# Optimization experiments

Hardware: AMD Instinct MI355X
Metric: run time of the kernel (lower is better)

The kernel has to match this reference:

```python
import jax, jax.numpy as jnp
import numpy as np

D_MODEL = 256
N_HEADS = 4
D_FF = 512
LN_EPS = 1e-5


def _ln(x, g, b):
    mu = jnp.mean(x, axis=-1, keepdims=True)
    var = jnp.mean(jnp.square(x - mu), axis=-1, keepdims=True)
    return (x - mu) * jax.lax.rsqrt(var + LN_EPS) * g + b


def setup_inputs() -> dict:
    key = jax.random.key(0)
    ks = jax.random.split(key, 12)
    d, h, f = D_MODEL, N_HEADS, D_FF
    s = 0.02
    return {
        "x": jax.random.normal(ks[0], (8, 2048, d), jnp.float32),
        # per-head Q/K/V projections: each head maps d_model -> d_model
        "Wq": jax.random.normal(ks[1], (h, d, d), jnp.float32) * s,
        "bq": jnp.zeros((h, d), jnp.float32),
        "Wk": jax.random.normal(ks[2], (h, d, d), jnp.float32) * s,
        "bk": jnp.zeros((h, d), jnp.float32),
        "Wv": jax.random.normal(ks[3], (h, d, d), jnp.float32) * s,
        "bv": jnp.zeros((h, d), jnp.float32),
        # output projection: (n_heads*d_model) -> d_model
        "Wo": jax.random.normal(ks[4], (h * d, d), jnp.float32) * s,
        "bo": jnp.zeros((d,), jnp.float32),
        # LayerNorms
        "g1": jnp.ones((d,), jnp.float32),
        "be1": jnp.zeros((d,), jnp.float32),
        "g2": jnp.ones((d,), jnp.float32),
        "be2": jnp.zeros((d,), jnp.float32),
        # FFN
        "W1": jax.random.normal(ks[5], (d, f), jnp.float32) * s,
        "bf1": jnp.zeros((f,), jnp.float32),
        "W2": jax.random.normal(ks[6], (f, d), jnp.float32) * s,
        "bf2": jnp.zeros((d,), jnp.float32),
    }


def reference(x, Wq, bq, Wk, bk, Wv, bv, Wo, bo, g1, be1, g2, be2, W1, bf1, W2, bf2):
    # Pre-norm attention block (dropout is identity at inference)
    xn = _ln(x, g1, be1)  # [b,s,d]
    q = jnp.einsum("bsd,hde->bhse", xn, Wq) + bq[None, :, None, :]
    k = jnp.einsum("bsd,hde->bhse", xn, Wk) + bk[None, :, None, :]
    v = jnp.einsum("bsd,hde->bhse", xn, Wv) + bv[None, :, None, :]
    scale = q.shape[-1] ** -0.5  # per-head dim == d_model here
    scores = jax.nn.softmax(jnp.einsum("bhse,bhte->bhst", q, k) * scale, axis=-1)
    attn = jnp.einsum("bhst,bhte->bhse", scores, v)  # [b,h,s,d]
    b, h, s, d = attn.shape
    cat = jnp.transpose(attn, (0, 2, 1, 3)).reshape(b, s, h * d)  # concat heads
    x = x + cat @ Wo + bo
    # Pre-norm FFN block
    xn = _ln(x, g2, be2)
    x = x + jax.nn.relu(xn @ W1 + bf1) @ W2 + bf2
    return x
```

## Files before the change

kernel.cpp:

```cpp
#include <hip/hip_runtime.h>

typedef __bf16 bf16x8 __attribute__((ext_vector_type(8)));
typedef float  f32x4  __attribute__((ext_vector_type(4)));
typedef float  f32x16 __attribute__((ext_vector_type(16)));

__device__ __forceinline__ unsigned short f2b(float f) {
    union { float f; unsigned int v; } c; c.f = f;
    unsigned int u = c.v;
    unsigned int r = u + 0x7FFFu + ((u >> 16) & 1u);
    return (unsigned short)(r >> 16);
}
__device__ __forceinline__ f32x4 mfma16(bf16x8 a, bf16x8 b, f32x4 c) {
    return __builtin_amdgcn_mfma_f32_16x16x32_bf16(a, b, c, 0, 0, 0);
}
__device__ __forceinline__ f32x16 mfma32(bf16x8 a, bf16x8 b, f32x16 c) {
    return __builtin_amdgcn_mfma_f32_32x32x16_bf16(a, b, c, 0, 0, 0);
}
__device__ __forceinline__ unsigned cvtpk(float a, float b) {
    unsigned r;
    asm("v_cvt_pk_bf16_f32 %0, %1, %2" : "=v"(r) : "v"(a), "v"(b));
    return r;
}

#define BB 8
#define SS 2048
#define DD 256
#define HH 4
#define FF 512
#define MM (BB * SS)

__global__ __launch_bounds__(256) void transpose_f32_kernel(
    const float* __restrict__ in, unsigned short* __restrict__ out,
    int inS, int outS, long long inZa, long long inZb, int zmod, long long outZ,
    float scale)
{
    __shared__ unsigned short T[64][72];
    const int z = blockIdx.z;
    in  += (long long)(z / zmod) * inZa + (long long)(z % zmod) * inZb;
    out += (long long)z * outZ;
    const int r0 = blockIdx.x * 64, c0 = blockIdx.y * 64;
    const int tid = threadIdx.x;
    const int row = tid >> 3;
    const int col = (tid & 7) * 8;
#pragma unroll
    for (int c = 0; c < 2; ++c) {
        int rr = c * 32 + row;
        const float4 a = *reinterpret_cast<const float4*>(&in[(long long)(r0 + rr) * inS + c0 + col]);
        const float4 b = *reinterpret_cast<const float4*>(&in[(long long)(r0 + rr) * inS + c0 + col + 4]);
        alignas(16) unsigned short t[8] = {
            f2b(a.x * scale), f2b(a.y * scale), f2b(a.z * scale), f2b(a.w * scale),
            f2b(b.x * scale), f2b(b.y * scale), f2b(b.z * scale), f2b(b.w * scale) };
        *reinterpret_cast<uint4*>(&T[rr][col]) = *reinterpret_cast<const uint4*>(t);
    }
    __syncthreads();
#pragma unroll
    for (int c = 0; c < 2; ++c) {
        int orow = c * 32 + row;
        alignas(16) unsigned short tmp[8];
#pragma unroll
        for (int j = 0; j < 8; ++j) tmp[j] = T[col + j][orow];
        *reinterpret_cast<uint4*>(&out[(long long)(c0 + orow) * outS + r0 + col]) =
            *reinterpret_cast<const uint4*>(tmp);
    }
}

__global__ __launch_bounds__(256) void bias_concat_kernel(
    const float* __restrict__ bq, const float* __restrict__ bk,
    const float* __restrict__ bv, float* __restrict__ qkb, float* __restrict__ vb)
{
    const int i = blockIdx.x * 256 + threadIdx.x;
    if (i < 1024)       qkb[i] = bq[i] * 0.0625f;
    else if (i < 2048)  qkb[i] = bk[i - 1024];
    else                vb[i - 2048] = bv[i - 2048];
}

__global__ __launch_bounds__(256) void ln_kernel(
    const float* __restrict__ in, const float* __restrict__ g,
    const float* __restrict__ bta, unsigned short* __restrict__ out)
{
    const int tid  = threadIdx.x;
    const int wave = tid >> 6, lane = tid & 63;
    const int row  = blockIdx.x * 4 + wave;
    const float4 v = reinterpret_cast<const float4*>(in)[(long long)row * 64 + lane];
    float x[4] = { v.x, v.y, v.z, v.w };
    float s = x[0] + x[1] + x[2] + x[3];
    float q = x[0]*x[0] + x[1]*x[1] + x[2]*x[2] + x[3]*x[3];
#pragma unroll
    for (int off = 1; off < 64; off <<= 1) {
        s += __shfl_xor(s, off);
        q += __shfl_xor(q, off);
    }
    const float mean = s * (1.0f / 256.0f);
    const float var  = q * (1.0f / 256.0f) - mean * mean;
    const float rs   = rsqrtf(var + 1e-5f);
    const float4 gv = reinterpret_cast<const float4*>(g)[lane];
    const float4 bv = reinterpret_cast<const float4*>(bta)[lane];
    unsigned short y[4];
    y[0] = f2b((x[0] - mean) * rs * gv.x + bv.x);
    y[1] = f2b((x[1] - mean) * rs * gv.y + bv.y);
    y[2] = f2b((x[2] - mean) * rs * gv.z + bv.z);
    y[3] = f2b((x[3] - mean) * rs * gv.w + bv.w);
    uint2 o;
    o.x = (unsigned int)y[0] | ((unsigned int)y[1] << 16);
    o.y = (unsigned int)y[2] | ((unsigned int)y[3] << 16);
    reinterpret_cast<uint2*>(out)[(long long)row * 64 + lane] = o;
}

template <bool RELU, int RES, bool OUTBF, int NS, bool VT>
__global__ __launch_bounds__(256) void gemm_kernel(
    const unsigned short* __restrict__ A, const unsigned short* __restrict__ BT,
    const float* __restrict__ bias, const float* __restrict__ res,
    void* __restrict__ out, int M, int N, int K)
{
    __shared__ unsigned short As[128 * 40];
    __shared__ unsigned short Bs[(NS == 4 ? 128 : 64) * 40];
    const int tid  = threadIdx.x;
    const int wave = tid >> 6, lane = tid & 63;
    const int quad = lane >> 4, l16 = lane & 15;
    const int wm = wave >> 1, wn = wave & 1;
    const int WN = NS * 16;
    const int m0 = blockIdx.x * 128, n0 = blockIdx.y * (2 * WN);

    f32x4 acc[4][NS];
#pragma unroll
    for (int i = 0; i < 4; ++i)
#pragma unroll
        for (int j = 0; j < NS; ++j) acc[i][j] = (f32x4){0.f, 0.f, 0.f, 0.f};

    const int srow = tid >> 2;
    const int scol = (tid & 3) * 8;

    for (int k0 = 0; k0 < K; k0 += 32) {
        __syncthreads();
#pragma unroll
        for (int c = 0; c < 2; ++c) {
            const int r = c * 64 + srow;
            *reinterpret_cast<uint4*>(&As[r * 40 + scol]) =
                *reinterpret_cast<const uint4*>(&A[(long long)(m0 + r) * K + k0 + scol]);
        }
        {
            *reinterpret_cast<uint4*>(&Bs[srow * 40 + scol]) =
                *reinterpret_cast<const uint4*>(&BT[(long long)(n0 + srow) * K + k0 + scol]);
            if (NS == 4) {
                const int r = 64 + srow;
                *reinterpret_cast<uint4*>(&Bs[r * 40 + scol]) =
                    *reinterpret_cast<const uint4*>(&BT[(long long)(n0 + r) * K + k0 + scol]);
            }
        }
        __syncthreads();
        bf16x8 af[4], bf[NS];
#pragma unroll
        for (int ms = 0; ms < 4; ++ms)
            af[ms] = *reinterpret_cast<const bf16x8*>(&As[(wm * 64 + ms * 16 + l16) * 40 + quad * 8]);
#pragma unroll
        for (int ns = 0; ns < NS; ++ns)
            bf[ns] = *reinterpret_cast<const bf16x8*>(&Bs[(wn * WN + ns * 16 + l16) * 40 + quad * 8]);
#pragma unroll
        for (int ms = 0; ms < 4; ++ms)
#pragma unroll
            for (int ns = 0; ns < NS; ++ns)
                acc[ms][ns] = mfma16(af[ms], bf[ns], acc[ms][ns]);
    }

#pragma unroll
    for (int ms = 0; ms < 4; ++ms) {
#pragma unroll
        for (int ns = 0; ns < NS; ++ns) {
            const int cg = n0 + wn * WN + ns * 16 + l16;
            const float bvc = VT ? 0.f : bias[cg];
#pragma unroll
            for (int r = 0; r < 4; ++r) {
                const int rg = m0 + wm * 64 + ms * 16 + quad * 4 + r;
                float v = acc[ms][ns][r] + (VT ? bias[rg] : bvc);
                if (RELU)   v = fmaxf(v, 0.0f);
                if (RES == 1)
                    v += res[(long long)rg * N + cg];
                if (VT) {
                    const long long oaddr =
                        (long long)((cg >> 11) * 4 + (rg >> 8)) * 524288 +
                        (long long)(rg & 255) * 2048 + (cg & 2047);
                    reinterpret_cast<unsigned short*>(out)[oaddr] = f2b(v);
                } else if (OUTBF) {
                    reinterpret_cast<unsigned short*>(out)[(long long)rg * N + cg] = f2b(v);
                } else {
                    reinterpret_cast<float*>(out)[(long long)rg * N + cg] = v;
                }
            }
        }
    }
}

__global__ __launch_bounds__(256, 2) void attn_kernel(
    const unsigned short* __restrict__ QK, const unsigned short* __restrict__ Vt,
    unsigned short* __restrict__ Cat)
{
    __shared__ __align__(16) unsigned short Ks[2][32 * 264];
    __shared__ __align__(16) unsigned short Vs[2][256 * 40];
    const int tid  = threadIdx.x;
    const int wave = tid >> 6, lane = tid & 63;
    const int l32 = lane & 31, half = lane >> 5;
    const int by = blockIdx.x;
    const int h = by & 3, b = by >> 2;
    const int q0 = blockIdx.y * 128;
    const unsigned short* Qb = QK + (long long)b * SS * 2048 + h * 256;
    const unsigned short* Kb = Qb + 1024;
    const unsigned short* vbase = Vt + (long long)by * DD * SS;

    bf16x8 qf[16];
    {
        const unsigned short* qrow = Qb + (long long)(q0 + wave * 32 + l32) * 2048 + half * 8;
#pragma unroll
        for (int kb = 0; kb < 16; ++kb)
            qf[kb] = *reinterpret_cast<const bf16x8*>(qrow + kb * 16);
    }

    f32x16 o[8];
#pragma unroll
    for (int i = 0; i < 8; ++i)
#pragma unroll
        for (int r = 0; r < 16; ++r) o[i][r] = 0.f;
    float lsum = 0.f;

    const int krow = tid >> 3;
    const int kcol = (tid & 7) * 8;
    const int ve   = tid >> 2;
    const int vtf  = (tid & 3) * 8;

    uint4 kreg[4], vreg[4];
#pragma unroll
    for (int c = 0; c < 4; ++c)
        kreg[c] = *reinterpret_cast<const uint4*>(&Kb[(long long)krow * 2048 + kcol + c * 64]);
#pragma unroll
    for (int c = 0; c < 4; ++c)
        vreg[c] = *reinterpret_cast<const uint4*>(&vbase[(long long)(ve + c * 64) * SS + vtf]);
#pragma unroll
    for (int c = 0; c < 4; ++c)
        *reinterpret_cast<uint4*>(&Ks[0][krow * 264 + kcol + c * 64]) = kreg[c];
#pragma unroll
    for (int c = 0; c < 4; ++c)
        *reinterpret_cast<uint4*>(&Vs[0][(ve + c * 64) * 40 + vtf]) = vreg[c];
    __syncthreads();

    for (int t = 0; t < 64; ++t) {
        const int cur = t & 1;
        if (t < 63) {
            const int t1 = (t + 1) * 32;
#pragma unroll
            for (int c = 0; c < 4; ++c)
                kreg[c] = *reinterpret_cast<const uint4*>(&Kb[(long long)(t1 + krow) * 2048 + kcol + c * 64]);
#pragma unroll
            for (int c = 0; c < 4; ++c)
                vreg[c] = *reinterpret_cast<const uint4*>(&vbase[(long long)(ve + c * 64) * SS + t1 + vtf]);
        }

        f32x16 sc0, sc1;
#pragma unroll
        for (int r = 0; r < 16; ++r) { sc0[r] = 0.f; sc1[r] = 0.f; }
        __builtin_amdgcn_s_setprio(1);
#pragma unroll
        for (int kb = 0; kb < 8; ++kb) {
            bf16x8 kf0 = *reinterpret_cast<const bf16x8*>(&Ks[cur][l32 * 264 + (2 * kb) * 16 + half * 8]);
            bf16x8 kf1 = *reinterpret_cast<const bf16x8*>(&Ks[cur][l32 * 264 + (2 * kb + 1) * 16 + half * 8]);
            sc0 = mfma32(kf0, qf[2 * kb], sc0);
            sc1 = mfma32(kf1, qf[2 * kb + 1], sc1);
        }
        __builtin_amdgcn_s_setprio(0);

        float p[16];
#pragma unroll
        for (int r = 0; r < 16; ++r) {
            p[r] = __expf(sc0[r] + sc1[r]);
            lsum += p[r];
        }

        unsigned pk[8];
#pragma unroll
        for (int i = 0; i < 8; ++i) pk[i] = cvtpk(p[2 * i], p[2 * i + 1]);
        union { bf16x8 v; unsigned u[4]; } A0, A1;
        {
            auto r = __builtin_amdgcn_permlane32_swap(pk[0], pk[2], false, false);
            A0.u[0] = r[0]; A0.u[2] = r[1];
        }
        {
            auto r = __builtin_amdgcn_permlane32_swap(pk[1], pk[3], false, false);
            A0.u[1] = r[0]; A0.u[3] = r[1];
        }
        {
            auto r = __builtin_amdgcn_permlane32_swap(pk[4], pk[6], false, false);
            A1.u[0] = r[0]; A1.u[2] = r[1];
        }
        {
            auto r = __builtin_amdgcn_permlane32_swap(pk[5], pk[7], false, false);
            A1.u[1] = r[0]; A1.u[3] = r[1];
        }

        __builtin_amdgcn_s_setprio(1);
#pragma unroll
        for (int et = 0; et < 8; ++et) {
            bf16x8 vf0 = *reinterpret_cast<const bf16x8*>(&Vs[cur][(et * 32 + l32) * 40 + half * 8]);
            bf16x8 vf1 = *reinterpret_cast<const bf16x8*>(&Vs[cur][(et * 32 + l32) * 40 + 16 + half * 8]);
            o[et] = mfma32(A0.v, vf0, o[et]);
            o[et] = mfma32(A1.v, vf1, o[et]);
        }
        __builtin_amdgcn_s_setprio(0);

        if (t < 63) {
            const int nxt = cur ^ 1;
#pragma unroll
            for (int c = 0; c < 4; ++c)
                *reinterpret_cast<uint4*>(&Ks[nxt][krow * 264 + kcol + c * 64]) = kreg[c];
#pragma unroll
            for (int c = 0; c < 4; ++c)
                *reinterpret_cast<uint4*>(&Vs[nxt][(ve + c * 64) * 40 + vtf]) = vreg[c];
            __syncthreads();
        }
    }

    lsum += __shfl_xor(lsum, 32);
    const float inv = 1.0f / lsum;
    float invr[16];
#pragma unroll
    for (int r = 0; r < 16; ++r)
        invr[r] = __shfl(inv, (r & 3) + 8 * (r >> 2) + 4 * half);

    const int rowb = b * SS + q0 + wave * 32;
#pragma unroll
    for (int et = 0; et < 8; ++et) {
        const int cg = h * 256 + et * 32 + l32;
#pragma unroll
        for (int r = 0; r < 16; ++r) {
            const int row = (r & 3) + 8 * (r >> 2) + 4 * half;
            Cat[(long long)(rowb + row) * (HH * DD) + cg] = f2b(o[et][r] * invr[r]);
        }
    }
}

extern "C" void kernel_launch(void* const* d_in, const int* in_sizes, int n_in,
                              void* d_out, int out_size, void* d_ws, size_t ws_size,
                              hipStream_t stream)
{
    const float* x   = (const float*)d_in[0];
    const float* Wq  = (const float*)d_in[1];
    const float* bq  = (const float*)d_in[2];
    const float* Wk  = (const float*)d_in[3];
    const float* bk  = (const float*)d_in[4];
    const float* Wv  = (const float*)d_in[5];
    const float* bv  = (const float*)d_in[6];
    const float* Wo  = (const float*)d_in[7];
    const float* bo  = (const float*)d_in[8];
    const float* g1  = (const float*)d_in[9];
    const float* be1 = (const float*)d_in[10];
    const float* g2  = (const float*)d_in[11];
    const float* be2 = (const float*)d_in[12];
    const float* W1  = (const float*)d_in[13];
    const float* bf1 = (const float*)d_in[14];
    const float* W2  = (const float*)d_in[15];
    const float* bf2 = (const float*)d_in[16];
    float* out = (float*)d_out;

    char* ws = (char*)d_ws;
    unsigned short* xn1  = (unsigned short*)(ws + 0);
    unsigned short* qk   = (unsigned short*)(ws + 8388608);
    unsigned short* cat  = (unsigned short*)(ws + 75497472);
    unsigned short* vt   = (unsigned short*)(ws + 109051904);
    unsigned short* wqkT = (unsigned short*)(ws + 142606336);
    unsigned short* wvT  = (unsigned short*)(ws + 143654912);
    unsigned short* woT  = (unsigned short*)(ws + 144179200);
    unsigned short* w1T  = (unsigned short*)(ws + 144703488);
    unsigned short* w2T  = (unsigned short*)(ws + 144965632);
    float*          qkb  = (float*)(ws + 145227776);
    float*          vb   = (float*)(ws + 145235968);
    float*          xmid = (float*)(ws + 8388608);
    unsigned short* xn2  = (unsigned short*)(ws + 25165824);
    unsigned short* mid  = (unsigned short*)(ws + 33554432);

    transpose_f32_kernel<<<dim3(4, 4, 4),  256, 0, stream>>>(Wq, wqkT,          256,  256, 0, 65536, 4, 65536, 0.0625f);
    transpose_f32_kernel<<<dim3(4, 4, 4),  256, 0, stream>>>(Wk, wqkT + 262144, 256,  256, 0, 65536, 4, 65536, 1.0f);
    transpose_f32_kernel<<<dim3(4, 4, 4),  256, 0, stream>>>(Wv, wvT,           256,  256, 0, 65536, 4, 65536, 1.0f);
    transpose_f32_kernel<<<dim3(16, 4, 1), 256, 0, stream>>>(Wo, woT,           256, 1024, 0, 0, 4, 0, 1.0f);
    transpose_f32_kernel<<<dim3(4, 8, 1),  256, 0, stream>>>(W1, w1T,           512,  256, 0, 0, 4, 0, 1.0f);
    transpose_f32_kernel<<<dim3(8, 4, 1),  256, 0, stream>>>(W2, w2T,           256,  512, 0, 0, 4, 0, 1.0f);
    bias_concat_kernel<<<dim3(12), 256, 0, stream>>>(bq, bk, bv, qkb, vb);

    ln_kernel<<<dim3(4096), 256, 0, stream>>>(x, g1, be1, xn1);

    gemm_kernel<false, 0, true, 4, false><<<dim3(128, 16), 256, 0, stream>>>(
        xn1, wqkT, qkb, nullptr, qk, MM, 2048, 256);
    gemm_kernel<false, 0, true, 4, true><<<dim3(8, 128), 256, 0, stream>>>(
        wvT, xn1, vb, nullptr, vt, 1024, MM, 256);

    attn_kernel<<<dim3(32, 16), 256, 0, stream>>>(qk, vt, cat);

    gemm_kernel<false, 1, false, 2, false><<<dim3(128, 4), 256, 0, stream>>>(
        cat, woT, bo, x, xmid, MM, 256, 1024);

    ln_kernel<<<dim3(4096), 256, 0, stream>>>(xmid, g2, be2, xn2);

    gemm_kernel<true, 0, true, 2, false><<<dim3(128, 8), 256, 0, stream>>>(
        xn2, w1T, bf1, nullptr, mid, MM, 512, 256);

    gemm_kernel<false, 1, false, 2, false><<<dim3(128, 4), 256, 0, stream>>>(
        mid, w2T, bf2, xmid, out, MM, 256, 512);

    (void)in_sizes; (void)n_in; (void)out_size; (void)ws_size;
}
```

Baseline: 363.4 us.

## Software-pipeline attention QK^T one tile ahead and fold log2e into Q scale

Restructures the attention key loop so the score MMA for tile t+1 is issued before the softmax and PV MMA of tile t. Two score accumulators alternate, the loop is unrolled by two with a macro, and global prefetch now runs two tiles ahead. The Q weights and bias are also prescaled by log2(e) so exp2f replaces __expf. The aim is to overlap exp/convert/permute work with MFMA and LDS latency, at the cost of more registers and a restructured barrier placement.

```diff
diff --git a/kernel.cpp b/kernel.cpp
--- a/kernel.cpp
+++ b/kernel.cpp
@@ -28,6 +28,7 @@
 #define HH 4
 #define FF 512
 #define MM (BB * SS)
+#define QSCALE (0.0625f * 1.44269504088896340736f)
 
 __global__ __launch_bounds__(256) void transpose_f32_kernel(
     const float* __restrict__ in, unsigned short* __restrict__ out,
@@ -69,7 +70,7 @@
     const float* __restrict__ bv, float* __restrict__ qkb, float* __restrict__ vb)
 {
     const int i = blockIdx.x * 256 + threadIdx.x;
-    if (i < 1024)       qkb[i] = bq[i] * 0.0625f;
+    if (i < 1024)       qkb[i] = bq[i] * QSCALE;
     else if (i < 2048)  qkb[i] = bk[i - 1024];
     else                vb[i - 2048] = bv[i - 2048];
 }
@@ -241,79 +242,103 @@
         *reinterpret_cast<uint4*>(&Vs[0][(ve + c * 64) * 40 + vtf]) = vreg[c];
     __syncthreads();
 
-    for (int t = 0; t < 64; ++t) {
-        const int cur = t & 1;
-        if (t < 63) {
-            const int t1 = (t + 1) * 32;
-#pragma unroll
-            for (int c = 0; c < 4; ++c)
-                kreg[c] = *reinterpret_cast<const uint4*>(&Kb[(long long)(t1 + krow) * 2048 + kcol + c * 64]);
-#pragma unroll
-            for (int c = 0; c < 4; ++c)
-                vreg[c] = *reinterpret_cast<const uint4*>(&vbase[(long long)(ve + c * 64) * SS + t1 + vtf]);
-        }
-
-        f32x16 sc0, sc1;
-#pragma unroll
-        for (int r = 0; r < 16; ++r) { sc0[r] = 0.f; sc1[r] = 0.f; }
+    f32x16 scA, scB;
+    {
+#pragma unroll
+        for (int r = 0; r < 16; ++r) scA[r] = 0.f;
         __builtin_amdgcn_s_setprio(1);
 #pragma unroll
-        for (int kb = 0; kb < 8; ++kb) {
-            bf16x8 kf0 = *reinterpret_cast<const bf16x8*>(&Ks[cur][l32 * 264 + (2 * kb) * 16 + half * 8]);
-            bf16x8 kf1 = *reinterpret_cast<const bf16x8*>(&Ks[cur][l32 * 264 + (2 * kb + 1) * 16 + half * 8]);
-            sc0 = mfma32(kf0, qf[2 * kb], sc0);
-            sc1 = mfma32(kf1, qf[2 * kb + 1], sc1);
+        for (int kb = 0; kb < 16; ++kb) {
+            bf16x8 kf = *reinterpret_cast<const bf16x8*>(&Ks[0][l32 * 264 + kb * 16 + half * 8]);
+            scA = mfma32(kf, qf[kb], scA);
         }
         __builtin_amdgcn_s_setprio(0);
-
+#pragma unroll
+        for (int c = 0; c < 4; ++c)
+            kreg[c] = *reinterpret_cast<const uint4*>(&Kb[(long long)(32 + krow) * 2048 + kcol + c * 64]);
+#pragma unroll
+        for (int c = 0; c < 4; ++c)
+            vreg[c] = *reinterpret_cast<const uint4*>(&vbase[(long long)(ve + c * 64) * SS + 32 + vtf]);
+    }
+
+#define ATTN_BODY(SCC, SCN, T, CUR, NXT)                                                        \
+    {                                                                                           \
+        _Pragma("unroll")                                                                       \
+        for (int c = 0; c < 4; ++c)                                                             \
+            *reinterpret_cast<uint4*>(&Ks[NXT][krow * 264 + kcol + c * 64]) = kreg[c];          \
+        __syncthreads();                                                                        \
+        _Pragma("unroll")                                                                       \
+        for (int c = 0; c < 4; ++c)                                                             \
+            *reinterpret_cast<uint4*>(&Vs[NXT][(ve + c * 64) * 40 + vtf]) = vreg[c];            \
+        _Pragma("unroll")                                                                       \
+        for (int r = 0; r < 16; ++r) SCN[r] = 0.f;                                              \
+        __builtin_amdgcn_s_setprio(1);                                                          \
+        _Pragma("unroll")                                                                       \
+        for (int kb = 0; kb < 16; ++kb) {                                                       \
+            bf16x8 kf = *reinterpret_cast<const bf16x8*>(&Ks[NXT][l32 * 264 + kb * 16 + half * 8]); \
+            SCN = mfma32(kf, qf[kb], SCN);                                                      \
+        }                                                                                       \
+        __builtin_amdgcn_s_setprio(0);                                                          \
+        float p[16];                                                                            \
+        _Pragma("unroll")                                                                       \
+        for (int r = 0; r < 16; ++r) { p[r] = exp2f(SCC[r]); lsum += p[r]; }                    \
+        unsigned pk[8];                                                                         \
+        _Pragma("unroll")                                                                       \
+        for (int i = 0; i < 8; ++i) pk[i] = cvtpk(p[2 * i], p[2 * i + 1]);                      \
+        union { bf16x8 v; unsigned u[4]; } A0, A1;                                              \
+        { auto rr = __builtin_amdgcn_permlane32_swap(pk[0], pk[2], false, false); A0.u[0] = rr[0]; A0.u[2] = rr[1]; } \
+        { auto rr = __builtin_amdgcn_permlane32_swap(pk[1], pk[3], false, false); A0.u[1] = rr[0]; A0.u[3] = rr[1]; } \
+        { auto rr = __builtin_amdgcn_permlane32_swap(pk[4], pk[6], false, false); A1.u[0] = rr[0]; A1.u[2] = rr[1]; } \
+        { auto rr = __builtin_amdgcn_permlane32_swap(pk[5], pk[7], false, false); A1.u[1] = rr[0]; A1.u[3] = rr[1]; } \
+        {                                                                                       \
+            const int t2 = ((T) + 2 <= 63 ? (T) + 2 : 63) * 32;                                 \
+            _Pragma("unroll")                                                                   \
+            for (int c = 0; c < 4; ++c)                                                         \
+                kreg[c] = *reinterpret_cast<const uint4*>(&Kb[(long long)(t2 + krow) * 2048 + kcol + c * 64]); \
+            _Pragma("unroll")                                                                   \
+            for (int c = 0; c < 4; ++c)                                                         \
+                vreg[c] = *reinterpret_cast<const uint4*>(&vbase[(long long)(ve + c * 64) * SS + t2 + vtf]); \
+        }                                                                                       \
+        __builtin_amdgcn_s_setprio(1);                                                          \
+        _Pragma("unroll")                                                                       \
+        for (int et = 0; et < 8; ++et) {                                                        \
+            bf16x8 vf0 = *reinterpret_cast<const bf16x8*>(&Vs[CUR][(et * 32 + l32) * 40 + half * 8]);      \
+            bf16x8 vf1 = *reinterpret_cast<const bf16x8*>(&Vs[CUR][(et * 32 + l32) * 40 + 16 + half * 8]); \
+            o[et] = mfma32(A0.v, vf0, o[et]);                                                   \
+            o[et] = mfma32(A1.v, vf1, o[et]);                                                   \
+        }                                                                                       \
+        __builtin_amdgcn_s_setprio(0);                                                          \
+    }
+
+    for (int t = 0; t < 62; t += 2) {
+        ATTN_BODY(scA, scB, t, 0, 1);
+        ATTN_BODY(scB, scA, t + 1, 1, 0);
+    }
+    ATTN_BODY(scA, scB, 62, 0, 1);
+#undef ATTN_BODY
+
+    __syncthreads();
+    {
         float p[16];
 #pragma unroll
-        for (int r = 0; r < 16; ++r) {
-            p[r] = __expf(sc0[r] + sc1[r]);
-            lsum += p[r];
-        }
-
+        for (int r = 0; r < 16; ++r) { p[r] = exp2f(scB[r]); lsum += p[r]; }
         unsigned pk[8];
 #pragma unroll
         for (int i = 0; i < 8; ++i) pk[i] = cvtpk(p[2 * i], p[2 * i + 1]);
         union { bf16x8 v; unsigned u[4]; } A0, A1;
-        {
-            auto r = __builtin_amdgcn_permlane32_swap(pk[0], pk[2], false, false);
-            A0.u[0] = r[0]; A0.u[2] = r[1];
-        }
-        {
-            auto r = __builtin_amdgcn_permlane32_swap(pk[1], pk[3], false, false);
-            A0.u[1] = r[0]; A0.u[3] = r[1];
-        }
-        {
-            auto r = __builtin_amdgcn_permlane32_swap(pk[4], pk[6], false, false);
-            A1.u[0] = r[0]; A1.u[2] = r[1];
-        }
-        {
-            auto r = __builtin_amdgcn_permlane32_swap(pk[5], pk[7], false, false);
-            A1.u[1] = r[0]; A1.u[3] = r[1];
-        }
-
+        { auto rr = __builtin_amdgcn_permlane32_swap(pk[0], pk[2], false, false); A0.u[0] = rr[0]; A0.u[2] = rr[1]; }
+        { auto rr = __builtin_amdgcn_permlane32_swap(pk[1], pk[3], false, false); A0.u[1] = rr[0]; A0.u[3] = rr[1]; }
+        { auto rr = __builtin_amdgcn_permlane32_swap(pk[4], pk[6], false, false); A1.u[0] = rr[0]; A1.u[2] = rr[1]; }
+        { auto rr = __builtin_amdgcn_permlane32_swap(pk[5], pk[7], false, false); A1.u[1] = rr[0]; A1.u[3] = rr[1]; }
         __builtin_amdgcn_s_setprio(1);
 #pragma unroll
         for (int et = 0; et < 8; ++et) {
-            bf16x8 vf0 = *reinterpret_cast<const bf16x8*>(&Vs[cur][(et * 32 + l32) * 40 + half * 8]);
-            bf16x8 vf1 = *reinterpret_cast<const bf16x8*>(&Vs[cur][(et * 32 + l32) * 40 + 16 + half * 8]);
+            bf16x8 vf0 = *reinterpret_cast<const bf16x8*>(&Vs[1][(et * 32 + l32) * 40 + half * 8]);
+            bf16x8 vf1 = *reinterpret_cast<const bf16x8*>(&Vs[1][(et * 32 + l32) * 40 + 16 + half * 8]);
             o[et] = mfma32(A0.v, vf0, o[et]);
             o[et] = mfma32(A1.v, vf1, o[et]);
         }
         __builtin_amdgcn_s_setprio(0);
-
-        if (t < 63) {
-            const int nxt = cur ^ 1;
-#pragma unroll
-            for (int c = 0; c < 4; ++c)
-                *reinterpret_cast<uint4*>(&Ks[nxt][krow * 264 + kcol + c * 64]) = kreg[c];
-#pragma unroll
-            for (int c = 0; c < 4; ++c)
-                *reinterpret_cast<uint4*>(&Vs[nxt][(ve + c * 64) * 40 + vtf]) = vreg[c];
-            __syncthreads();
-        }
     }
 
     lsum += __shfl_xor(lsum, 32);
@@ -374,7 +399,7 @@
     unsigned short* xn2  = (unsigned short*)(ws + 25165824);
     unsigned short* mid  = (unsigned short*)(ws + 33554432);
 
-    transpose_f32_kernel<<<dim3(4, 4, 4),  256, 0, stream>>>(Wq, wqkT,          256,  256, 0, 65536, 4, 65536, 0.0625f);
+    transpose_f32_kernel<<<dim3(4, 4, 4),  256, 0, stream>>>(Wq, wqkT,          256,  256, 0, 65536, 4, 65536, QSCALE);
     transpose_f32_kernel<<<dim3(4, 4, 4),  256, 0, stream>>>(Wk, wqkT + 262144, 256,  256, 0, 65536, 4, 65536, 1.0f);
     transpose_f32_kernel<<<dim3(4, 4, 4),  256, 0, stream>>>(Wv, wvT,           256,  256, 0, 65536, 4, 65536, 1.0f);
     transpose_f32_kernel<<<dim3(16, 4, 1), 256, 0, stream>>>(Wo, woT,           256, 1024, 0, 0, 4, 0, 1.0f);
```

New measurement: 937.0 us. 2.58x slower.

## Load V fragments directly from global memory and fold log2e into Q scale

Applied to the files above, without the earlier changes.

The attention kernel no longer stages V tiles in shared memory. Each wave reads its V MFMA fragments straight from global memory (the transposed V layout) and interleaves those loads with the PV MFMAs, which removes half the LDS traffic and shared footprint. The log2(e) factor is folded into the Q weight and bias scaling, so the softmax uses exp2f instead of __expf. In exchange, every wave re-reads V from global or L2, so the four waves each fetch the same data, and load latency now sits on the critical path between MFMAs.

```diff
diff --git a/kernel.cpp b/kernel.cpp
--- a/kernel.cpp
+++ b/kernel.cpp
@@ -28,6 +28,7 @@
 #define HH 4
 #define FF 512
 #define MM (BB * SS)
+#define QSCALE (0.0625f * 1.44269504088896340736f)
 
 __global__ __launch_bounds__(256) void transpose_f32_kernel(
     const float* __restrict__ in, unsigned short* __restrict__ out,
@@ -69,7 +70,7 @@
     const float* __restrict__ bv, float* __restrict__ qkb, float* __restrict__ vb)
 {
     const int i = blockIdx.x * 256 + threadIdx.x;
-    if (i < 1024)       qkb[i] = bq[i] * 0.0625f;
+    if (i < 1024)       qkb[i] = bq[i] * QSCALE;
     else if (i < 2048)  qkb[i] = bk[i - 1024];
     else                vb[i - 2048] = bv[i - 2048];
 }
@@ -195,7 +196,6 @@
     unsigned short* __restrict__ Cat)
 {
     __shared__ __align__(16) unsigned short Ks[2][32 * 264];
-    __shared__ __align__(16) unsigned short Vs[2][256 * 40];
     const int tid  = threadIdx.x;
     const int wave = tid >> 6, lane = tid & 63;
     const int l32 = lane & 31, half = lane >> 5;
@@ -223,34 +223,26 @@
 
     const int krow = tid >> 3;
     const int kcol = (tid & 7) * 8;
-    const int ve   = tid >> 2;
-    const int vtf  = (tid & 3) * 8;
-
-    uint4 kreg[4], vreg[4];
+
+#define VLD(ET, O16) (*reinterpret_cast<const bf16x8*>(                                   \
+        &vbase[(long long)((ET) * 32 + l32) * SS + t0 + (O16) + half * 8]))
+
+    uint4 kreg[4];
 #pragma unroll
     for (int c = 0; c < 4; ++c)
         kreg[c] = *reinterpret_cast<const uint4*>(&Kb[(long long)krow * 2048 + kcol + c * 64]);
 #pragma unroll
     for (int c = 0; c < 4; ++c)
-        vreg[c] = *reinterpret_cast<const uint4*>(&vbase[(long long)(ve + c * 64) * SS + vtf]);
-#pragma unroll
-    for (int c = 0; c < 4; ++c)
         *reinterpret_cast<uint4*>(&Ks[0][krow * 264 + kcol + c * 64]) = kreg[c];
-#pragma unroll
-    for (int c = 0; c < 4; ++c)
-        *reinterpret_cast<uint4*>(&Vs[0][(ve + c * 64) * 40 + vtf]) = vreg[c];
     __syncthreads();
 
     for (int t = 0; t < 64; ++t) {
         const int cur = t & 1;
+        const int t0 = t * 32;
         if (t < 63) {
-            const int t1 = (t + 1) * 32;
 #pragma unroll
             for (int c = 0; c < 4; ++c)
-                kreg[c] = *reinterpret_cast<const uint4*>(&Kb[(long long)(t1 + krow) * 2048 + kcol + c * 64]);
-#pragma unroll
-            for (int c = 0; c < 4; ++c)
-                vreg[c] = *reinterpret_cast<const uint4*>(&vbase[(long long)(ve + c * 64) * SS + t1 + vtf]);
+                kreg[c] = *reinterpret_cast<const uint4*>(&Kb[(long long)(t0 + 32 + krow) * 2048 + kcol + c * 64]);
         }
 
         f32x16 sc0, sc1;
@@ -266,42 +258,38 @@
         }
         __builtin_amdgcn_s_setprio(0);
 
-        float p[16];
-#pragma unroll
-        for (int r = 0; r < 16; ++r) {
-            p[r] = __expf(sc0[r] + sc1[r]);
-            lsum += p[r];
-        }
+        bf16x8 va0 = VLD(0, 0), va1 = VLD(0, 16);
+        bf16x8 vb0 = VLD(1, 0), vb1 = VLD(1, 16);
 
         unsigned pk[8];
 #pragma unroll
-        for (int i = 0; i < 8; ++i) pk[i] = cvtpk(p[2 * i], p[2 * i + 1]);
+        for (int i = 0; i < 8; ++i) {
+            const float pa = exp2f(sc0[2 * i]     + sc1[2 * i]);
+            const float pb = exp2f(sc0[2 * i + 1] + sc1[2 * i + 1]);
+            lsum += pa + pb;
+            pk[i] = cvtpk(pa, pb);
+        }
         union { bf16x8 v; unsigned u[4]; } A0, A1;
-        {
-            auto r = __builtin_amdgcn_permlane32_swap(pk[0], pk[2], false, false);
-            A0.u[0] = r[0]; A0.u[2] = r[1];
-        }
-        {
-            auto r = __builtin_amdgcn_permlane32_swap(pk[1], pk[3], false, false);
-            A0.u[1] = r[0]; A0.u[3] = r[1];
-        }
-        {
-            auto r = __builtin_amdgcn_permlane32_swap(pk[4], pk[6], false, false);
-            A1.u[0] = r[0]; A1.u[2] = r[1];
-        }
-        {
-            auto r = __builtin_amdgcn_permlane32_swap(pk[5], pk[7], false, false);
-            A1.u[1] = r[0]; A1.u[3] = r[1];
-        }
+        { auto rr = __builtin_amdgcn_permlane32_swap(pk[0], pk[2], false, false); A0.u[0] = rr[0]; A0.u[2] = rr[1]; }
+        { auto rr = __builtin_amdgcn_permlane32_swap(pk[1], pk[3], false, false); A0.u[1] = rr[0]; A0.u[3] = rr[1]; }
+        { auto rr = __builtin_amdgcn_permlane32_swap(pk[4], pk[6], false, false); A1.u[0] = rr[0]; A1.u[2] = rr[1]; }
+        { auto rr = __builtin_amdgcn_permlane32_swap(pk[5], pk[7], false, false); A1.u[1] = rr[0]; A1.u[3] = rr[1]; }
 
         __builtin_amdgcn_s_setprio(1);
-#pragma unroll
-        for (int et = 0; et < 8; ++et) {
-            bf16x8 vf0 = *reinterpret_cast<const bf16x8*>(&Vs[cur][(et * 32 + l32) * 40 + half * 8]);
-            bf16x8 vf1 = *reinterpret_cast<const bf16x8*>(&Vs[cur][(et * 32 + l32) * 40 + 16 + half * 8]);
-            o[et] = mfma32(A0.v, vf0, o[et]);
-            o[et] = mfma32(A1.v, vf1, o[et]);
-        }
+        o[0] = mfma32(A0.v, va0, o[0]); o[0] = mfma32(A1.v, va1, o[0]);
+        va0 = VLD(2, 0); va1 = VLD(2, 16);
+        o[1] = mfma32(A0.v, vb0, o[1]); o[1] = mfma32(A1.v, vb1, o[1]);
+        vb0 = VLD(3, 0); vb1 = VLD(3, 16);
+        o[2] = mfma32(A0.v, va0, o[2]); o[2] = mfma32(A1.v, va1, o[2]);
+        va0 = VLD(4, 0); va1 = VLD(4, 16);
+        o[3] = mfma32(A0.v, vb0, o[3]); o[3] = mfma32(A1.v, vb1, o[3]);
+        vb0 = VLD(5, 0); vb1 = VLD(5, 16);
+        o[4] = mfma32(A0.v, va0, o[4]); o[4] = mfma32(A1.v, va1, o[4]);
+        va0 = VLD(6, 0); va1 = VLD(6, 16);
+        o[5] = mfma32(A0.v, vb0, o[5]); o[5] = mfma32(A1.v, vb1, o[5]);
+        vb0 = VLD(7, 0); vb1 = VLD(7, 16);
+        o[6] = mfma32(A0.v, va0, o[6]); o[6] = mfma32(A1.v, va1, o[6]);
+        o[7] = mfma32(A0.v, vb0, o[7]); o[7] = mfma32(A1.v, vb1, o[7]);
         __builtin_amdgcn_s_setprio(0);
 
         if (t < 63) {
@@ -309,12 +297,10 @@
 #pragma unroll
             for (int c = 0; c < 4; ++c)
                 *reinterpret_cast<uint4*>(&Ks[nxt][krow * 264 + kcol + c * 64]) = kreg[c];
-#pragma unroll
-            for (int c = 0; c < 4; ++c)
-                *reinterpret_cast<uint4*>(&Vs[nxt][(ve + c * 64) * 40 + vtf]) = vreg[c];
             __syncthreads();
         }
     }
+#undef VLD
 
     lsum += __shfl_xor(lsum, 32);
     const float inv = 1.0f / lsum;
@@ -374,7 +360,7 @@
     unsigned short* xn2  = (unsigned short*)(ws + 25165824);
     unsigned short* mid  = (unsigned short*)(ws + 33554432);
 
-    transpose_f32_kernel<<<dim3(4, 4, 4),  256, 0, stream>>>(Wq, wqkT,          256,  256, 0, 65536, 4, 65536, 0.0625f);
+    transpose_f32_kernel<<<dim3(4, 4, 4),  256, 0, stream>>>(Wq, wqkT,          256,  256, 0, 65536, 4, 65536, QSCALE);
     transpose_f32_kernel<<<dim3(4, 4, 4),  256, 0, stream>>>(Wk, wqkT + 262144, 256,  256, 0, 65536, 4, 65536, 1.0f);
     transpose_f32_kernel<<<dim3(4, 4, 4),  256, 0, stream>>>(Wv, wvT,           256,  256, 0, 65536, 4, 65536, 1.0f);
     transpose_f32_kernel<<<dim3(16, 4, 1), 256, 0, stream>>>(Wo, woT,           256, 1024, 0, 0, 4, 0, 1.0f);
```

New measurement: 504.9 us. 39.0% more time.

## Double-buffer GEMM shared tiles and fold log2e into Q scale for exp2

Applied to the files above, without the earlier changes.

The GEMM kernel now keeps two shared-memory buffers for the A and B tiles. It prefetches the next K-slice into registers while the MFMAs run on the current slice, which leaves one barrier per iteration instead of two. In attention, log2(e) is folded into the Q weight and bias scale so softmax can use exp2f directly. The two split score accumulators are merged into one chain of 16 dependent MFMAs. The double buffering doubles LDS use per block, and the single accumulator chain adds MFMA dependency latency.

```diff
diff --git a/kernel.cpp b/kernel.cpp
--- a/kernel.cpp
+++ b/kernel.cpp
@@ -28,6 +28,7 @@
 #define HH 4
 #define FF 512
 #define MM (BB * SS)
+#define QSCALE (0.0625f * 1.44269504088896340736f)
 
 __global__ __launch_bounds__(256) void transpose_f32_kernel(
     const float* __restrict__ in, unsigned short* __restrict__ out,
@@ -69,7 +70,7 @@
     const float* __restrict__ bv, float* __restrict__ qkb, float* __restrict__ vb)
 {
     const int i = blockIdx.x * 256 + threadIdx.x;
-    if (i < 1024)       qkb[i] = bq[i] * 0.0625f;
+    if (i < 1024)       qkb[i] = bq[i] * QSCALE;
     else if (i < 2048)  qkb[i] = bk[i - 1024];
     else                vb[i - 2048] = bv[i - 2048];
 }
@@ -112,8 +113,8 @@
     const float* __restrict__ bias, const float* __restrict__ res,
     void* __restrict__ out, int M, int N, int K)
 {
-    __shared__ unsigned short As[128 * 40];
-    __shared__ unsigned short Bs[(NS == 4 ? 128 : 64) * 40];
+    __shared__ unsigned short As[2][128 * 40];
+    __shared__ unsigned short Bs[2][(NS == 4 ? 128 : 64) * 40];
     const int tid  = threadIdx.x;
     const int wave = tid >> 6, lane = tid & 63;
     const int quad = lane >> 4, l16 = lane & 15;
@@ -130,36 +131,57 @@
     const int srow = tid >> 2;
     const int scol = (tid & 3) * 8;
 
-    for (int k0 = 0; k0 < K; k0 += 32) {
-        __syncthreads();
-#pragma unroll
-        for (int c = 0; c < 2; ++c) {
-            const int r = c * 64 + srow;
-            *reinterpret_cast<uint4*>(&As[r * 40 + scol]) =
-                *reinterpret_cast<const uint4*>(&A[(long long)(m0 + r) * K + k0 + scol]);
-        }
-        {
-            *reinterpret_cast<uint4*>(&Bs[srow * 40 + scol]) =
-                *reinterpret_cast<const uint4*>(&BT[(long long)(n0 + srow) * K + k0 + scol]);
-            if (NS == 4) {
-                const int r = 64 + srow;
-                *reinterpret_cast<uint4*>(&Bs[r * 40 + scol]) =
-                    *reinterpret_cast<const uint4*>(&BT[(long long)(n0 + r) * K + k0 + scol]);
-            }
-        }
-        __syncthreads();
+    uint4 areg[2], breg[2];
+#pragma unroll
+    for (int c = 0; c < 2; ++c)
+        areg[c] = *reinterpret_cast<const uint4*>(&A[(long long)(m0 + c * 64 + srow) * K + scol]);
+    breg[0] = *reinterpret_cast<const uint4*>(&BT[(long long)(n0 + srow) * K + scol]);
+    if (NS == 4)
+        breg[1] = *reinterpret_cast<const uint4*>(&BT[(long long)(n0 + 64 + srow) * K + scol]);
+#pragma unroll
+    for (int c = 0; c < 2; ++c)
+        *reinterpret_cast<uint4*>(&As[0][(c * 64 + srow) * 40 + scol]) = areg[c];
+    *reinterpret_cast<uint4*>(&Bs[0][srow * 40 + scol]) = breg[0];
+    if (NS == 4)
+        *reinterpret_cast<uint4*>(&Bs[0][(64 + srow) * 40 + scol]) = breg[1];
+    __syncthreads();
+
+    const int nk = K >> 5;
+    for (int it = 0; it < nk; ++it) {
+        const int cur = it & 1;
+        if (it + 1 < nk) {
+            const int k0 = (it + 1) * 32;
+#pragma unroll
+            for (int c = 0; c < 2; ++c)
+                areg[c] = *reinterpret_cast<const uint4*>(&A[(long long)(m0 + c * 64 + srow) * K + k0 + scol]);
+            breg[0] = *reinterpret_cast<const uint4*>(&BT[(long long)(n0 + srow) * K + k0 + scol]);
+            if (NS == 4)
+                breg[1] = *reinterpret_cast<const uint4*>(&BT[(long long)(n0 + 64 + srow) * K + k0 + scol]);
+        }
+
         bf16x8 af[4], bf[NS];
 #pragma unroll
         for (int ms = 0; ms < 4; ++ms)
-            af[ms] = *reinterpret_cast<const bf16x8*>(&As[(wm * 64 + ms * 16 + l16) * 40 + quad * 8]);
+            af[ms] = *reinterpret_cast<const bf16x8*>(&As[cur][(wm * 64 + ms * 16 + l16) * 40 + quad * 8]);
 #pragma unroll
         for (int ns = 0; ns < NS; ++ns)
-            bf[ns] = *reinterpret_cast<const bf16x8*>(&Bs[(wn * WN + ns * 16 + l16) * 40 + quad * 8]);
+            bf[ns] = *reinterpret_cast<const bf16x8*>(&Bs[cur][(wn * WN + ns * 16 + l16) * 40 + quad * 8]);
 #pragma unroll
         for (int ms = 0; ms < 4; ++ms)
 #pragma unroll
             for (int ns = 0; ns < NS; ++ns)
                 acc[ms][ns] = mfma16(af[ms], bf[ns], acc[ms][ns]);
+
+        if (it + 1 < nk) {
+            const int nxt = cur ^ 1;
+#pragma unroll
+            for (int c = 0; c < 2; ++c)
+                *reinterpret_cast<uint4*>(&As[nxt][(c * 64 + srow) * 40 + scol]) = areg[c];
+            *reinterpret_cast<uint4*>(&Bs[nxt][srow * 40 + scol]) = breg[0];
+            if (NS == 4)
+                *reinterpret_cast<uint4*>(&Bs[nxt][(64 + srow) * 40 + scol]) = breg[1];
+            __syncthreads();
+        }
     }
 
 #pragma unroll
@@ -253,23 +275,21 @@
                 vreg[c] = *reinterpret_cast<const uint4*>(&vbase[(long long)(ve + c * 64) * SS + t1 + vtf]);
         }
 
-        f32x16 sc0, sc1;
-#pragma unroll
-        for (int r = 0; r < 16; ++r) { sc0[r] = 0.f; sc1[r] = 0.f; }
+        f32x16 sc;
+#pragma unroll
+        for (int r = 0; r < 16; ++r) sc[r] = 0.f;
         __builtin_amdgcn_s_setprio(1);
 #pragma unroll
-        for (int kb = 0; kb < 8; ++kb) {
-            bf16x8 kf0 = *reinterpret_cast<const bf16x8*>(&Ks[cur][l32 * 264 + (2 * kb) * 16 + half * 8]);
-            bf16x8 kf1 = *reinterpret_cast<const bf16x8*>(&Ks[cur][l32 * 264 + (2 * kb + 1) * 16 + half * 8]);
-            sc0 = mfma32(kf0, qf[2 * kb], sc0);
-            sc1 = mfma32(kf1, qf[2 * kb + 1], sc1);
+        for (int kb = 0; kb < 16; ++kb) {
+            bf16x8 kf = *reinterpret_cast<const bf16x8*>(&Ks[cur][l32 * 264 + kb * 16 + half * 8]);
+            sc = mfma32(kf, qf[kb], sc);
         }
         __builtin_amdgcn_s_setprio(0);
 
         float p[16];
 #pragma unroll
         for (int r = 0; r < 16; ++r) {
-            p[r] = __expf(sc0[r] + sc1[r]);
+            p[r] = exp2f(sc[r]);
             lsum += p[r];
         }
 
@@ -277,22 +297,10 @@
 #pragma unroll
         for (int i = 0; i < 8; ++i) pk[i] = cvtpk(p[2 * i], p[2 * i + 1]);
         union { bf16x8 v; unsigned u[4]; } A0, A1;
-        {
-            auto r = __builtin_amdgcn_permlane32_swap(pk[0], pk[2], false, false);
-            A0.u[0] = r[0]; A0.u[2] = r[1];
-        }
-        {
-            auto r = __builtin_amdgcn_permlane32_swap(pk[1], pk[3], false, false);
-            A0.u[1] = r[0]; A0.u[3] = r[1];
-        }
-        {
-            auto r = __builtin_amdgcn_permlane32_swap(pk[4], pk[6], false, false);
-            A1.u[0] = r[0]; A1.u[2] = r[1];
-        }
-        {
-            auto r = __builtin_amdgcn_permlane32_swap(pk[5], pk[7], false, false);
-            A1.u[1] = r[0]; A1.u[3] = r[1];
-        }
+        { auto rr = __builtin_amdgcn_permlane32_swap(pk[0], pk[2], false, false); A0.u[0] = rr[0]; A0.u[2] = rr[1]; }
+        { auto rr = __builtin_amdgcn_permlane32_swap(pk[1], pk[3], false, false); A0.u[1] = rr[0]; A0.u[3] = rr[1]; }
+        { auto rr = __builtin_amdgcn_permlane32_swap(pk[4], pk[6], false, false); A1.u[0] = rr[0]; A1.u[2] = rr[1]; }
+        { auto rr = __builtin_amdgcn_permlane32_swap(pk[5], pk[7], false, false); A1.u[1] = rr[0]; A1.u[3] = rr[1]; }
 
         __builtin_amdgcn_s_setprio(1);
 #pragma unroll
@@ -374,7 +382,7 @@
     unsigned short* xn2  = (unsigned short*)(ws + 25165824);
     unsigned short* mid  = (unsigned short*)(ws + 33554432);
 
-    transpose_f32_kernel<<<dim3(4, 4, 4),  256, 0, stream>>>(Wq, wqkT,          256,  256, 0, 65536, 4, 65536, 0.0625f);
+    transpose_f32_kernel<<<dim3(4, 4, 4),  256, 0, stream>>>(Wq, wqkT,          256,  256, 0, 65536, 4, 65536, QSCALE);
     transpose_f32_kernel<<<dim3(4, 4, 4),  256, 0, stream>>>(Wk, wqkT + 262144, 256,  256, 0, 65536, 4, 65536, 1.0f);
     transpose_f32_kernel<<<dim3(4, 4, 4),  256, 0, stream>>>(Wv, wvT,           256,  256, 0, 65536, 4, 65536, 1.0f);
     transpose_f32_kernel<<<dim3(16, 4, 1), 256, 0, stream>>>(Wo, woT,           256, 1024, 0, 0, 4, 0, 1.0f);
```

Measured after the change: 503.9 us. 1.39x slower.
